# Kernel tuning notes

Hardware: AMD Instinct MI355X
Metric: run time of the kernel (lower is better)

Reference implementation:

```python
import jax, jax.numpy as jnp
import numpy as np

H, W, C_IN, C_ADD = 721, 1440, 78, 8
N_NODES, K = 5882, 128
DAY_OF_YEAR = 182.5  # module default time_of_year
LN_EPS = 1e-5        # haiku LayerNorm default
NORM_EPS = 1e-7


def setup_inputs() -> dict:
    key = jax.random.key(0)
    ks = jax.random.split(key, 4)
    return {
        "var_grid": jax.random.normal(ks[0], (H, W, C_IN), dtype=jnp.float32),
        "nearby_idx": jax.random.randint(ks[1], (N_NODES, K), 0, H * W),
        "input_means": jnp.zeros((C_IN + C_ADD,), jnp.float32),
        "input_stds": jnp.ones((C_IN + C_ADD,), jnp.float32),
        "W1": jax.random.normal(ks[2], (C_IN + C_ADD, 256), dtype=jnp.float32) * 0.1,
        "b1": jnp.zeros((256,), jnp.float32),
        "ln_scale": jnp.ones((256,), jnp.float32),
        "ln_offset": jnp.zeros((256,), jnp.float32),
        "W2": jax.random.normal(ks[3], (256, 256), dtype=jnp.float32) * 0.1,
        "b2": jnp.zeros((256,), jnp.float32),
    }


def _additional_features(h, w):
    # 8 extra channels: sin/cos of lat/lon, normalized day-of-year, 3 zero pads
    lat = jnp.linspace(-90.0, 90.0, h)
    lon = jnp.linspace(0.0, 360.0, w)
    lat2d = jnp.broadcast_to(lat[:, None], (h, w))
    lon2d = jnp.broadcast_to(lon[None, :], (h, w))
    lat_r, lon_r = jnp.radians(lat2d), jnp.radians(lon2d)
    day = jnp.float32(DAY_OF_YEAR / 365.0)
    z = jnp.zeros((h, w), jnp.float32)
    return jnp.stack([
        jnp.sin(lat_r), jnp.cos(lat_r), jnp.sin(lon_r), jnp.cos(lon_r),
        jnp.full((h, w), day, jnp.float32), z, z, z,
    ], axis=-1)  # [H, W, 8]


def reference(var_grid, nearby_idx, input_means, input_stds,
              W1, b1, ln_scale, ln_offset, W2, b2):
    h, w, c = var_grid.shape
    add = _additional_features(h, w)                       # [H, W, 8]
    flat = jnp.concatenate([var_grid, add], -1).reshape(h * w, c + C_ADD)
    gathered = flat[nearby_idx]                            # [N, K, 86] irregular gather
    x = (gathered - input_means) / (input_stds + NORM_EPS)
    hidden = jax.nn.relu(jnp.einsum('nkc,cd->nkd', x, W1) + b1)
    mu = hidden.mean(-1, keepdims=True)
    var = hidden.var(-1, keepdims=True)
    hidden = (hidden - mu) * jax.lax.rsqrt(var + LN_EPS) * ln_scale + ln_offset
    nodes = jnp.einsum('nkd,de->nke', hidden, W2) + b2     # [N, K, 256]
    return nodes
```

## Files before the change

kernel.cpp:

```cpp
#include <hip/hip_runtime.h>
#include <hip/hip_bf16.h>
#include <math.h>

#define GH 721
#define GW 1440
#define C_IN 78
#define NNODES 5882
#define KNEIGH 128
#define M_TOTAL (NNODES * KNEIGH)
#define TM 64
#define NBLOCKS (M_TOTAL / TM)

typedef __attribute__((ext_vector_type(8))) short bf16x8;
typedef __attribute__((ext_vector_type(4))) float f32x4;

__device__ __forceinline__ unsigned short f2bf(float x) {
    __hip_bfloat16 b = __float2bfloat16(x);
    union { __hip_bfloat16 h; unsigned short u; } cv; cv.h = b; return cv.u;
}

__global__ void prep_kernel(const float* __restrict__ W1, const float* __restrict__ W2,
                            const float* __restrict__ means, const float* __restrict__ stds,
                            const float* __restrict__ b1, const float* __restrict__ lnS,
                            const float* __restrict__ lnO, const float* __restrict__ b2,
                            unsigned short* __restrict__ bp1, unsigned short* __restrict__ bp2,
                            float* __restrict__ latT, float* __restrict__ lonT,
                            float* __restrict__ b1p, float* __restrict__ K1,
                            float* __restrict__ K2)
{
    const int NB1 = 3 * 4 * 256 * 8;
    const int NB2 = 8 * 4 * 256 * 8;
    const int NTOT = NB1 + NB2 + GH + GW + 256;
    for (int e = blockIdx.x * blockDim.x + threadIdx.x; e < NTOT;
         e += gridDim.x * blockDim.x) {
        if (e < NB1) {
            int j = e & 7, c = (e >> 3) & 255, o = (e >> 11) & 3, s = e >> 13;
            int k = s * 32 + o * 8 + j;
            float v = 0.f;
            if (k < 82) v = W1[k * 256 + c] / (stds[k] + 1e-7f);
            bp1[e] = f2bf(v);
        } else if (e < NB1 + NB2) {
            int t = e - NB1;
            int j = t & 7, c = (t >> 3) & 255, o = (t >> 11) & 3, s = t >> 13;
            int k = s * 32 + o * 8 + j;
            bp2[t] = f2bf(W2[k * 256 + c] * lnS[k]);
        } else if (e < NB1 + NB2 + GH) {
            int h = e - NB1 - NB2;
            float r = (-90.f + 0.25f * (float)h) * 0.017453292519943295f;
            latT[2 * h]     = sinf(r);
            latT[2 * h + 1] = cosf(r);
        } else if (e < NB1 + NB2 + GH + GW) {
            int w = e - NB1 - NB2 - GH;
            float r = ((float)w * (360.f / 1439.f)) * 0.017453292519943295f;
            lonT[2 * w]     = sinf(r);
            lonT[2 * w + 1] = cosf(r);
        } else {
            int c = e - NB1 - NB2 - GH - GW;
            float acc = b1[c];
            #pragma unroll 1
            for (int k = 0; k < 86; ++k) {
                float inv = 1.f / (stds[k] + 1e-7f);
                float w = W1[k * 256 + c] * inv;
                acc -= means[k] * w;
                if (k == 82) acc += 0.5f * w;
            }
            b1p[c] = acc;
            float k1 = 0.f, k2 = 0.f;
            #pragma unroll 1
            for (int k = 0; k < 256; ++k) {
                float w = W2[k * 256 + c];
                k1 += lnS[k] * w;
                k2 += lnO[k] * w;
            }
            K1[c] = k1;
            K2[c] = k2 + b2[c];
        }
    }
}

__global__ __launch_bounds__(512, 4)
void fused_kernel(const float* __restrict__ var_grid, const int* __restrict__ idxs,
                  const unsigned short* __restrict__ bp1, const unsigned short* __restrict__ bp2,
                  const float* __restrict__ latT, const float* __restrict__ lonT,
                  const float* __restrict__ b1p, const float* __restrict__ K1,
                  const float* __restrict__ K2,
                  float* __restrict__ out)
{
    __shared__ __align__(16) char smem[TM * 256 * 2];
    __shared__ float red[2][4][TM];
    unsigned short* h_lds = (unsigned short*)smem;
    unsigned short (*x_lds)[104] = (unsigned short (*)[104])smem;

    const int q_ = 1470, r_ = 4;
    const int xcd = blockIdx.x & 7;
    const int ii  = blockIdx.x >> 3;
    const int swz = (xcd < r_ ? xcd * (q_ + 1) : r_ * (q_ + 1) + (xcd - r_) * q_) + ii;

    const int tid  = threadIdx.x;
    const int lane = tid & 63;
    const int wave = tid >> 6;
    const int wr   = wave >> 2;
    const int wc   = wave & 3;
    const int l15  = lane & 15;
    const int lg   = lane >> 4;
    const int wbase = wc * 64;
    const int rbase = wr * 32;
    const long block0 = (long)swz * TM;

    {
        const int row = tid >> 3, p = tid & 7;
        const int idx = idxs[block0 + row];
        const int hh = idx / GW;
        const int ww = idx - hh * GW;
        const float* src = var_grid + (long)idx * C_IN;
        float2 g[5], tl, tl2;
        #pragma unroll
        for (int t = 0; t < 5; ++t) {
            const int q = p + 8 * t;
            if (q < 39) g[t] = *(const float2*)(src + 2 * q);
        }
        tl.x  = latT[2 * hh]; tl.y  = latT[2 * hh + 1];
        tl2.x = lonT[2 * ww]; tl2.y = lonT[2 * ww + 1];
        unsigned int* xrow = (unsigned int*)&x_lds[row][0];
        #pragma unroll
        for (int t = 0; t < 6; ++t) {
            const int q = p + 8 * t;
            float v0, v1;
            if (q < 39)      { v0 = g[t].x; v1 = g[t].y; }
            else if (q == 39){ v0 = tl.x;  v1 = tl.y; }
            else if (q == 40){ v0 = tl2.x; v1 = tl2.y; }
            else             { v0 = 0.f; v1 = 0.f; }
            xrow[q] = ((unsigned int)f2bf(v1) << 16) | (unsigned int)f2bf(v0);
        }
    }

    float b1v[4];
    #pragma unroll
    for (int nf = 0; nf < 4; ++nf) b1v[nf] = b1p[wbase + nf * 16 + l15];
    __syncthreads();

    f32x4 acc[2][4];
    #pragma unroll
    for (int mf = 0; mf < 2; ++mf)
        #pragma unroll
        for (int nf = 0; nf < 4; ++nf) acc[mf][nf] = (f32x4){0.f, 0.f, 0.f, 0.f};

    #pragma unroll
    for (int s = 0; s < 3; ++s) {
        bf16x8 af[2], bw[4];
        #pragma unroll
        for (int nf = 0; nf < 4; ++nf)
            bw[nf] = *(const bf16x8*)(bp1 + ((size_t)((s * 4 + lg) * 256) + wbase + nf * 16 + l15) * 8);
        #pragma unroll
        for (int mf = 0; mf < 2; ++mf)
            af[mf] = *(const bf16x8*)&x_lds[rbase + mf * 16 + l15][s * 32 + lg * 8];
        #pragma unroll
        for (int mf = 0; mf < 2; ++mf)
            #pragma unroll
            for (int nf = 0; nf < 4; ++nf)
                acc[mf][nf] = __builtin_amdgcn_mfma_f32_16x16x32_bf16(af[mf], bw[nf], acc[mf][nf], 0, 0, 0);
    }

    __syncthreads();

    float sm[2][4], sq[2][4];
    #pragma unroll
    for (int mf = 0; mf < 2; ++mf)
        #pragma unroll
        for (int i = 0; i < 4; ++i) { sm[mf][i] = 0.f; sq[mf][i] = 0.f; }

    #pragma unroll
    for (int mf = 0; mf < 2; ++mf)
        #pragma unroll
        for (int nf = 0; nf < 4; ++nf)
            #pragma unroll
            for (int i = 0; i < 4; ++i) {
                float v = fmaxf(acc[mf][nf][i] + b1v[nf], 0.f);
                sm[mf][i] += v;
                sq[mf][i] += v * v;
                int row = rbase + mf * 16 + lg * 4 + i;
                int col = wbase + nf * 16 + l15;
                unsigned off = (unsigned)(row * 512 + col * 2);
                off ^= (unsigned)((row & 7) << 4);
                *(unsigned short*)((char*)h_lds + off) = f2bf(v);
            }

    #pragma unroll
    for (int m = 1; m < 16; m <<= 1)
        #pragma unroll
        for (int mf = 0; mf < 2; ++mf)
            #pragma unroll
            for (int i = 0; i < 4; ++i) {
                sm[mf][i] += __shfl_xor(sm[mf][i], m, 64);
                sq[mf][i] += __shfl_xor(sq[mf][i], m, 64);
            }

    if (l15 == 0) {
        #pragma unroll
        for (int mf = 0; mf < 2; ++mf)
            #pragma unroll
            for (int i = 0; i < 4; ++i) {
                int row = rbase + mf * 16 + lg * 4 + i;
                red[0][wc][row] = sm[mf][i];
                red[1][wc][row] = sq[mf][i];
            }
    }
    __syncthreads();

    #pragma unroll
    for (int mf = 0; mf < 2; ++mf)
        #pragma unroll
        for (int nf = 0; nf < 4; ++nf) acc[mf][nf] = (f32x4){0.f, 0.f, 0.f, 0.f};

    #pragma unroll
    for (int s = 0; s < 8; ++s) {
        bf16x8 af[2], bw[4];
        #pragma unroll
        for (int nf = 0; nf < 4; ++nf)
            bw[nf] = *(const bf16x8*)(bp2 + ((size_t)((s * 4 + lg) * 256) + wbase + nf * 16 + l15) * 8);
        #pragma unroll
        for (int mf = 0; mf < 2; ++mf) {
            int row = rbase + mf * 16 + l15;
            unsigned off = (unsigned)(row * 512 + (s * 32 + lg * 8) * 2);
            off ^= (unsigned)((row & 7) << 4);
            af[mf] = *(const bf16x8*)((char*)h_lds + off);
        }
        #pragma unroll
        for (int mf = 0; mf < 2; ++mf)
            #pragma unroll
            for (int nf = 0; nf < 4; ++nf)
                acc[mf][nf] = __builtin_amdgcn_mfma_f32_16x16x32_bf16(af[mf], bw[nf], acc[mf][nf], 0, 0, 0);
    }

    float K1v[4], K2v[4];
    #pragma unroll
    for (int nf = 0; nf < 4; ++nf) {
        int col = wbase + nf * 16 + l15;
        K1v[nf] = K1[col]; K2v[nf] = K2[col];
    }
    #pragma unroll
    for (int mf = 0; mf < 2; ++mf)
        #pragma unroll
        for (int i = 0; i < 4; ++i) {
            int row = rbase + mf * 16 + lg * 4 + i;
            float tot = red[0][0][row] + red[0][1][row] + red[0][2][row] + red[0][3][row];
            float tq  = red[1][0][row] + red[1][1][row] + red[1][2][row] + red[1][3][row];
            float mean = tot * (1.f / 256.f);
            float var  = tq * (1.f / 256.f) - mean * mean;
            float rs = rsqrtf(var + 1e-5f);
            long row_g = block0 + row;
            float* po = out + row_g * 256 + wbase;
            #pragma unroll
            for (int nf = 0; nf < 4; ++nf)
                po[nf * 16 + l15] = rs * (acc[mf][nf][i] - mean * K1v[nf]) + K2v[nf];
        }
}

extern "C" void kernel_launch(void* const* d_in, const int* in_sizes, int n_in,
                              void* d_out, int out_size, void* d_ws, size_t ws_size,
                              hipStream_t stream) {
    const float* var_grid = (const float*)d_in[0];
    const int*   idxs     = (const int*)d_in[1];
    const float* means    = (const float*)d_in[2];
    const float* stds     = (const float*)d_in[3];
    const float* W1       = (const float*)d_in[4];
    const float* b1       = (const float*)d_in[5];
    const float* lnS      = (const float*)d_in[6];
    const float* lnO      = (const float*)d_in[7];
    const float* W2       = (const float*)d_in[8];
    const float* b2       = (const float*)d_in[9];
    float* out = (float*)d_out;

    char* ws = (char*)d_ws;
    unsigned short* bp1 = (unsigned short*)ws;
    unsigned short* bp2 = (unsigned short*)(ws + 49152);
    float* latT = (float*)(ws + 180224);
    float* lonT = (float*)(ws + 186000);
    float* b1p  = (float*)(ws + 197520);
    float* K1   = (float*)(ws + 198544);
    float* K2   = (float*)(ws + 199568);

    prep_kernel<<<362, 256, 0, stream>>>(W1, W2, means, stds, b1, lnS, lnO, b2,
                                         bp1, bp2, latT, lonT, b1p, K1, K2);
    fused_kernel<<<NBLOCKS, 512, 0, stream>>>(var_grid, idxs, bp1, bp2, latT, lonT,
                                              b1p, K1, K2, out);
}
```

Before: 427.6 us.

## Make fused kernel persistent over four tiles with double-buffered gather prefetch

Each block now handles four 64-row tiles instead of one, with the XCD swizzle constants updated for the smaller grid. The irregular gather for the next tile is issued into registers during the current tile's GEMMs and packed into a second x buffer. The aim is to hide gather latency behind MFMA work and amortize block launch and bias loads. The cost is more LDS (separate x, h and reduction buffers) and more live registers, which may lower occupancy under launch_bounds(512,4).

```diff
diff --git a/kernel.cpp b/kernel.cpp
--- a/kernel.cpp
+++ b/kernel.cpp
@@ -9,7 +9,8 @@
 #define KNEIGH 128
 #define M_TOTAL (NNODES * KNEIGH)
 #define TM 64
-#define NBLOCKS (M_TOTAL / TM)
+#define TILES 4
+#define NBLOCKS (M_TOTAL / (TM * TILES))
 
 typedef __attribute__((ext_vector_type(8))) short bf16x8;
 typedef __attribute__((ext_vector_type(4))) float f32x4;
@@ -86,12 +87,11 @@
                   const float* __restrict__ K2,
                   float* __restrict__ out)
 {
-    __shared__ __align__(16) char smem[TM * 256 * 2];
-    __shared__ float red[2][4][TM];
-    unsigned short* h_lds = (unsigned short*)smem;
-    unsigned short (*x_lds)[104] = (unsigned short (*)[104])smem;
-
-    const int q_ = 1470, r_ = 4;
+    __shared__ __align__(16) unsigned short x_lds[2][TM][104];
+    __shared__ __align__(16) unsigned short h_lds[TM * 256];
+    __shared__ float red[2][2][4][TM];
+
+    const int q_ = 367, r_ = 5;
     const int xcd = blockIdx.x & 7;
     const int ii  = blockIdx.x >> 3;
     const int swz = (xcd < r_ ? xcd * (q_ + 1) : r_ * (q_ + 1) + (xcd - r_) * q_) + ii;
@@ -105,155 +105,170 @@
     const int lg   = lane >> 4;
     const int wbase = wc * 64;
     const int rbase = wr * 32;
-    const long block0 = (long)swz * TM;
-
-    {
-        const int row = tid >> 3, p = tid & 7;
-        const int idx = idxs[block0 + row];
+    const long block0 = (long)swz * (TM * TILES);
+
+    const int grow = tid >> 3, gp = tid & 7;
+
+    float2 g[5], tl, tl2;
+
+    auto issue = [&](int t) {
+        const int idx = idxs[block0 + t * TM + grow];
         const int hh = idx / GW;
         const int ww = idx - hh * GW;
         const float* src = var_grid + (long)idx * C_IN;
-        float2 g[5], tl, tl2;
-        #pragma unroll
-        for (int t = 0; t < 5; ++t) {
-            const int q = p + 8 * t;
-            if (q < 39) g[t] = *(const float2*)(src + 2 * q);
+        #pragma unroll
+        for (int u = 0; u < 5; ++u) {
+            const int q = gp + 8 * u;
+            if (q < 39) g[u] = *(const float2*)(src + 2 * q);
         }
         tl.x  = latT[2 * hh]; tl.y  = latT[2 * hh + 1];
         tl2.x = lonT[2 * ww]; tl2.y = lonT[2 * ww + 1];
-        unsigned int* xrow = (unsigned int*)&x_lds[row][0];
-        #pragma unroll
-        for (int t = 0; t < 6; ++t) {
-            const int q = p + 8 * t;
+    };
+    auto pack = [&](int buf) {
+        unsigned int* xrow = (unsigned int*)&x_lds[buf][grow][0];
+        #pragma unroll
+        for (int u = 0; u < 6; ++u) {
+            const int q = gp + 8 * u;
             float v0, v1;
-            if (q < 39)      { v0 = g[t].x; v1 = g[t].y; }
-            else if (q == 39){ v0 = tl.x;  v1 = tl.y; }
-            else if (q == 40){ v0 = tl2.x; v1 = tl2.y; }
-            else             { v0 = 0.f; v1 = 0.f; }
+            if (q < 39)       { v0 = g[u].x; v1 = g[u].y; }
+            else if (q == 39) { v0 = tl.x;  v1 = tl.y; }
+            else if (q == 40) { v0 = tl2.x; v1 = tl2.y; }
+            else              { v0 = 0.f; v1 = 0.f; }
             xrow[q] = ((unsigned int)f2bf(v1) << 16) | (unsigned int)f2bf(v0);
         }
-    }
-
+    };
+
+    issue(0);
     float b1v[4];
     #pragma unroll
     for (int nf = 0; nf < 4; ++nf) b1v[nf] = b1p[wbase + nf * 16 + l15];
-    __syncthreads();
-
-    f32x4 acc[2][4];
+    pack(0);
+
     #pragma unroll
-    for (int mf = 0; mf < 2; ++mf)
-        #pragma unroll
-        for (int nf = 0; nf < 4; ++nf) acc[mf][nf] = (f32x4){0.f, 0.f, 0.f, 0.f};
-
-    #pragma unroll
-    for (int s = 0; s < 3; ++s) {
-        bf16x8 af[2], bw[4];
-        #pragma unroll
-        for (int nf = 0; nf < 4; ++nf)
-            bw[nf] = *(const bf16x8*)(bp1 + ((size_t)((s * 4 + lg) * 256) + wbase + nf * 16 + l15) * 8);
-        #pragma unroll
-        for (int mf = 0; mf < 2; ++mf)
-            af[mf] = *(const bf16x8*)&x_lds[rbase + mf * 16 + l15][s * 32 + lg * 8];
-        #pragma unroll
-        for (int mf = 0; mf < 2; ++mf)
+    for (int t = 0; t < TILES; ++t) {
+        __syncthreads();
+
+        if (t + 1 < TILES) issue(t + 1);
+
+        f32x4 acc[2][4];
+        #pragma unroll
+        for (int mf = 0; mf < 2; ++mf)
+            #pragma unroll
+            for (int nf = 0; nf < 4; ++nf) acc[mf][nf] = (f32x4){0.f, 0.f, 0.f, 0.f};
+
+        #pragma unroll
+        for (int s = 0; s < 3; ++s) {
+            bf16x8 af[2], bw[4];
             #pragma unroll
             for (int nf = 0; nf < 4; ++nf)
-                acc[mf][nf] = __builtin_amdgcn_mfma_f32_16x16x32_bf16(af[mf], bw[nf], acc[mf][nf], 0, 0, 0);
-    }
-
-    __syncthreads();
-
-    float sm[2][4], sq[2][4];
-    #pragma unroll
-    for (int mf = 0; mf < 2; ++mf)
-        #pragma unroll
-        for (int i = 0; i < 4; ++i) { sm[mf][i] = 0.f; sq[mf][i] = 0.f; }
-
-    #pragma unroll
-    for (int mf = 0; mf < 2; ++mf)
-        #pragma unroll
-        for (int nf = 0; nf < 4; ++nf)
-            #pragma unroll
-            for (int i = 0; i < 4; ++i) {
-                float v = fmaxf(acc[mf][nf][i] + b1v[nf], 0.f);
-                sm[mf][i] += v;
-                sq[mf][i] += v * v;
-                int row = rbase + mf * 16 + lg * 4 + i;
-                int col = wbase + nf * 16 + l15;
-                unsigned off = (unsigned)(row * 512 + col * 2);
+                bw[nf] = *(const bf16x8*)(bp1 + ((size_t)((s * 4 + lg) * 256) + wbase + nf * 16 + l15) * 8);
+            #pragma unroll
+            for (int mf = 0; mf < 2; ++mf)
+                af[mf] = *(const bf16x8*)&x_lds[t & 1][rbase + mf * 16 + l15][s * 32 + lg * 8];
+            #pragma unroll
+            for (int mf = 0; mf < 2; ++mf)
+                #pragma unroll
+                for (int nf = 0; nf < 4; ++nf)
+                    acc[mf][nf] = __builtin_amdgcn_mfma_f32_16x16x32_bf16(af[mf], bw[nf], acc[mf][nf], 0, 0, 0);
+        }
+
+        float sm[2][4], sq[2][4];
+        #pragma unroll
+        for (int mf = 0; mf < 2; ++mf)
+            #pragma unroll
+            for (int i = 0; i < 4; ++i) { sm[mf][i] = 0.f; sq[mf][i] = 0.f; }
+
+        #pragma unroll
+        for (int mf = 0; mf < 2; ++mf)
+            #pragma unroll
+            for (int nf = 0; nf < 4; ++nf)
+                #pragma unroll
+                for (int i = 0; i < 4; ++i) {
+                    float v = fmaxf(acc[mf][nf][i] + b1v[nf], 0.f);
+                    sm[mf][i] += v;
+                    sq[mf][i] += v * v;
+                    int row = rbase + mf * 16 + lg * 4 + i;
+                    int col = wbase + nf * 16 + l15;
+                    unsigned off = (unsigned)(row * 512 + col * 2);
+                    off ^= (unsigned)((row & 7) << 4);
+                    *(unsigned short*)((char*)h_lds + off) = f2bf(v);
+                }
+
+        #pragma unroll
+        for (int m = 1; m < 16; m <<= 1)
+            #pragma unroll
+            for (int mf = 0; mf < 2; ++mf)
+                #pragma unroll
+                for (int i = 0; i < 4; ++i) {
+                    sm[mf][i] += __shfl_xor(sm[mf][i], m, 64);
+                    sq[mf][i] += __shfl_xor(sq[mf][i], m, 64);
+                }
+
+        if (l15 == 0) {
+            #pragma unroll
+            for (int mf = 0; mf < 2; ++mf)
+                #pragma unroll
+                for (int i = 0; i < 4; ++i) {
+                    int row = rbase + mf * 16 + lg * 4 + i;
+                    red[t & 1][0][wc][row] = sm[mf][i];
+                    red[t & 1][1][wc][row] = sq[mf][i];
+                }
+        }
+
+        if (t + 1 < TILES) pack((t + 1) & 1);
+
+        __syncthreads();
+
+        #pragma unroll
+        for (int mf = 0; mf < 2; ++mf)
+            #pragma unroll
+            for (int nf = 0; nf < 4; ++nf) acc[mf][nf] = (f32x4){0.f, 0.f, 0.f, 0.f};
+
+        #pragma unroll
+        for (int s = 0; s < 8; ++s) {
+            bf16x8 af[2], bw[4];
+            #pragma unroll
+            for (int nf = 0; nf < 4; ++nf)
+                bw[nf] = *(const bf16x8*)(bp2 + ((size_t)((s * 4 + lg) * 256) + wbase + nf * 16 + l15) * 8);
+            #pragma unroll
+            for (int mf = 0; mf < 2; ++mf) {
+                int row = rbase + mf * 16 + l15;
+                unsigned off = (unsigned)(row * 512 + (s * 32 + lg * 8) * 2);
                 off ^= (unsigned)((row & 7) << 4);
-                *(unsigned short*)((char*)h_lds + off) = f2bf(v);
+                af[mf] = *(const bf16x8*)((char*)h_lds + off);
             }
-
-    #pragma unroll
-    for (int m = 1; m < 16; m <<= 1)
-        #pragma unroll
-        for (int mf = 0; mf < 2; ++mf)
-            #pragma unroll
-            for (int i = 0; i < 4; ++i) {
-                sm[mf][i] += __shfl_xor(sm[mf][i], m, 64);
-                sq[mf][i] += __shfl_xor(sq[mf][i], m, 64);
-            }
-
-    if (l15 == 0) {
+            #pragma unroll
+            for (int mf = 0; mf < 2; ++mf)
+                #pragma unroll
+                for (int nf = 0; nf < 4; ++nf)
+                    acc[mf][nf] = __builtin_amdgcn_mfma_f32_16x16x32_bf16(af[mf], bw[nf], acc[mf][nf], 0, 0, 0);
+        }
+
+        float K1v[4], K2v[4];
+        #pragma unroll
+        for (int nf = 0; nf < 4; ++nf) {
+            int col = wbase + nf * 16 + l15;
+            K1v[nf] = K1[col]; K2v[nf] = K2[col];
+        }
         #pragma unroll
         for (int mf = 0; mf < 2; ++mf)
             #pragma unroll
             for (int i = 0; i < 4; ++i) {
                 int row = rbase + mf * 16 + lg * 4 + i;
-                red[0][wc][row] = sm[mf][i];
-                red[1][wc][row] = sq[mf][i];
+                float tot = red[t & 1][0][0][row] + red[t & 1][0][1][row]
+                          + red[t & 1][0][2][row] + red[t & 1][0][3][row];
+                float tq  = red[t & 1][1][0][row] + red[t & 1][1][1][row]
+                          + red[t & 1][1][2][row] + red[t & 1][1][3][row];
+                float mean = tot * (1.f / 256.f);
+                float var  = tq * (1.f / 256.f) - mean * mean;
+                float rs = rsqrtf(var + 1e-5f);
+                long row_g = block0 + t * TM + row;
+                float* po = out + row_g * 256 + wbase;
+                #pragma unroll
+                for (int nf = 0; nf < 4; ++nf)
+                    po[nf * 16 + l15] = rs * (acc[mf][nf][i] - mean * K1v[nf]) + K2v[nf];
             }
     }
-    __syncthreads();
-
-    #pragma unroll
-    for (int mf = 0; mf < 2; ++mf)
-        #pragma unroll
-        for (int nf = 0; nf < 4; ++nf) acc[mf][nf] = (f32x4){0.f, 0.f, 0.f, 0.f};
-
-    #pragma unroll
-    for (int s = 0; s < 8; ++s) {
-        bf16x8 af[2], bw[4];
-        #pragma unroll
-        for (int nf = 0; nf < 4; ++nf)
-            bw[nf] = *(const bf16x8*)(bp2 + ((size_t)((s * 4 + lg) * 256) + wbase + nf * 16 + l15) * 8);
-        #pragma unroll
-        for (int mf = 0; mf < 2; ++mf) {
-            int row = rbase + mf * 16 + l15;
-            unsigned off = (unsigned)(row * 512 + (s * 32 + lg * 8) * 2);
-            off ^= (unsigned)((row & 7) << 4);
-            af[mf] = *(const bf16x8*)((char*)h_lds + off);
-        }
-        #pragma unroll
-        for (int mf = 0; mf < 2; ++mf)
-            #pragma unroll
-            for (int nf = 0; nf < 4; ++nf)
-                acc[mf][nf] = __builtin_amdgcn_mfma_f32_16x16x32_bf16(af[mf], bw[nf], acc[mf][nf], 0, 0, 0);
-    }
-
-    float K1v[4], K2v[4];
-    #pragma unroll
-    for (int nf = 0; nf < 4; ++nf) {
-        int col = wbase + nf * 16 + l15;
-        K1v[nf] = K1[col]; K2v[nf] = K2[col];
-    }
-    #pragma unroll
-    for (int mf = 0; mf < 2; ++mf)
-        #pragma unroll
-        for (int i = 0; i < 4; ++i) {
-            int row = rbase + mf * 16 + lg * 4 + i;
-            float tot = red[0][0][row] + red[0][1][row] + red[0][2][row] + red[0][3][row];
-            float tq  = red[1][0][row] + red[1][1][row] + red[1][2][row] + red[1][3][row];
-            float mean = tot * (1.f / 256.f);
-            float var  = tq * (1.f / 256.f) - mean * mean;
-            float rs = rsqrtf(var + 1e-5f);
-            long row_g = block0 + row;
-            float* po = out + row_g * 256 + wbase;
-            #pragma unroll
-            for (int nf = 0; nf < 4; ++nf)
-                po[nf * 16 + l15] = rs * (acc[mf][nf][i] - mean * K1v[nf]) + K2v[nf];
-        }
 }
 
 extern "C" void kernel_launch(void* const* d_in, const int* in_sizes, int n_in,
```

Result: slower. 909.3 us (+112.7%).

## Split gather into separate kernel writing bf16 staging buffer before MLP

Applied to the files above, without the earlier changes.

Splits the fused gather+MLP kernel into a standalone gather kernel and an MLP kernel. The gather kernel writes bf16 rows padded to 96 columns into a workspace buffer, and the MLP kernel reads its A operand straight from global memory. The intent is to decouple the latency-bound irregular gather from the MFMA compute. The cost is an extra round trip of about 144 MB through HBM. A fallback keeps the fused path when the workspace is too small.

```diff
diff --git a/kernel.cpp b/kernel.cpp
--- a/kernel.cpp
+++ b/kernel.cpp
@@ -8,8 +8,6 @@
 #define NNODES 5882
 #define KNEIGH 128
 #define M_TOTAL (NNODES * KNEIGH)
-#define TM 64
-#define NBLOCKS (M_TOTAL / TM)
 
 typedef __attribute__((ext_vector_type(8))) short bf16x8;
 typedef __attribute__((ext_vector_type(4))) float f32x4;
@@ -78,23 +76,63 @@
     }
 }
 
+__global__ __launch_bounds__(256)
+void gather_kernel(const float* __restrict__ var_grid, const int* __restrict__ idxs,
+                   const float* __restrict__ latT, const float* __restrict__ lonT,
+                   unsigned short* __restrict__ xbuf)
+{
+    const long NU = (long)M_TOTAL * 12;
+    const int b = blockIdx.x;
+    const int swz = (b & 7) * 256 + (b >> 3);
+    for (long unit = (long)swz * 256 + threadIdx.x; unit < NU;
+         unit += (long)gridDim.x * 256) {
+        const int row = (int)(unit / 12);
+        const int u   = (int)(unit - (long)row * 12);
+        const int idx = idxs[row];
+        const float* src = var_grid + (long)idx * C_IN;
+        float v[8];
+        if (u < 9) {
+            #pragma unroll
+            for (int j = 0; j < 4; ++j) {
+                float2 t = *(const float2*)(src + u * 8 + 2 * j);
+                v[2 * j] = t.x; v[2 * j + 1] = t.y;
+            }
+        } else if (u == 9) {
+            #pragma unroll
+            for (int j = 0; j < 3; ++j) {
+                float2 t = *(const float2*)(src + 72 + 2 * j);
+                v[2 * j] = t.x; v[2 * j + 1] = t.y;
+            }
+            int hh = idx / GW;
+            v[6] = latT[2 * hh]; v[7] = latT[2 * hh + 1];
+        } else if (u == 10) {
+            int hh = idx / GW;
+            int ww = idx - hh * GW;
+            v[0] = lonT[2 * ww]; v[1] = lonT[2 * ww + 1];
+            #pragma unroll
+            for (int j = 2; j < 8; ++j) v[j] = 0.f;
+        } else {
+            #pragma unroll
+            for (int j = 0; j < 8; ++j) v[j] = 0.f;
+        }
+        uint4 o;
+        o.x = ((unsigned)f2bf(v[1]) << 16) | f2bf(v[0]);
+        o.y = ((unsigned)f2bf(v[3]) << 16) | f2bf(v[2]);
+        o.z = ((unsigned)f2bf(v[5]) << 16) | f2bf(v[4]);
+        o.w = ((unsigned)f2bf(v[7]) << 16) | f2bf(v[6]);
+        *(uint4*)(xbuf + (size_t)row * 96 + u * 8) = o;
+    }
+}
+
 __global__ __launch_bounds__(512, 4)
-void fused_kernel(const float* __restrict__ var_grid, const int* __restrict__ idxs,
-                  const unsigned short* __restrict__ bp1, const unsigned short* __restrict__ bp2,
-                  const float* __restrict__ latT, const float* __restrict__ lonT,
-                  const float* __restrict__ b1p, const float* __restrict__ K1,
-                  const float* __restrict__ K2,
-                  float* __restrict__ out)
+void mlp_kernel(const unsigned short* __restrict__ xbuf,
+                const unsigned short* __restrict__ bp1, const unsigned short* __restrict__ bp2,
+                const float* __restrict__ b1p, const float* __restrict__ K1,
+                const float* __restrict__ K2,
+                float* __restrict__ out)
 {
-    __shared__ __align__(16) char smem[TM * 256 * 2];
-    __shared__ float red[2][4][TM];
-    unsigned short* h_lds = (unsigned short*)smem;
-    unsigned short (*x_lds)[104] = (unsigned short (*)[104])smem;
-
-    const int q_ = 1470, r_ = 4;
-    const int xcd = blockIdx.x & 7;
-    const int ii  = blockIdx.x >> 3;
-    const int swz = (xcd < r_ ? xcd * (q_ + 1) : r_ * (q_ + 1) + (xcd - r_) * q_) + ii;
+    __shared__ __align__(16) unsigned short h_lds[64 * 256];
+    __shared__ float red[2][4][64];
 
     const int tid  = threadIdx.x;
     const int lane = tid & 63;
@@ -105,7 +143,155 @@
     const int lg   = lane >> 4;
     const int wbase = wc * 64;
     const int rbase = wr * 32;
-    const long block0 = (long)swz * TM;
+    const long block0 = (long)blockIdx.x * 64;
+
+    float b1v[4];
+    #pragma unroll
+    for (int nf = 0; nf < 4; ++nf) b1v[nf] = b1p[wbase + nf * 16 + l15];
+
+    f32x4 acc[2][4];
+    #pragma unroll
+    for (int mf = 0; mf < 2; ++mf)
+        #pragma unroll
+        for (int nf = 0; nf < 4; ++nf) acc[mf][nf] = (f32x4){0.f, 0.f, 0.f, 0.f};
+
+    #pragma unroll
+    for (int s = 0; s < 3; ++s) {
+        bf16x8 af[2], bw[4];
+        #pragma unroll
+        for (int nf = 0; nf < 4; ++nf)
+            bw[nf] = *(const bf16x8*)(bp1 + ((size_t)((s * 4 + lg) * 256) + wbase + nf * 16 + l15) * 8);
+        #pragma unroll
+        for (int mf = 0; mf < 2; ++mf)
+            af[mf] = *(const bf16x8*)(xbuf + (size_t)(block0 + rbase + mf * 16 + l15) * 96
+                                            + s * 32 + lg * 8);
+        #pragma unroll
+        for (int mf = 0; mf < 2; ++mf)
+            #pragma unroll
+            for (int nf = 0; nf < 4; ++nf)
+                acc[mf][nf] = __builtin_amdgcn_mfma_f32_16x16x32_bf16(af[mf], bw[nf], acc[mf][nf], 0, 0, 0);
+    }
+
+    float sm[2][4], sq[2][4];
+    #pragma unroll
+    for (int mf = 0; mf < 2; ++mf)
+        #pragma unroll
+        for (int i = 0; i < 4; ++i) { sm[mf][i] = 0.f; sq[mf][i] = 0.f; }
+
+    #pragma unroll
+    for (int mf = 0; mf < 2; ++mf)
+        #pragma unroll
+        for (int nf = 0; nf < 4; ++nf)
+            #pragma unroll
+            for (int i = 0; i < 4; ++i) {
+                float v = fmaxf(acc[mf][nf][i] + b1v[nf], 0.f);
+                sm[mf][i] += v;
+                sq[mf][i] += v * v;
+                int row = rbase + mf * 16 + lg * 4 + i;
+                int col = wbase + nf * 16 + l15;
+                unsigned off = (unsigned)(row * 512 + col * 2);
+                off ^= (unsigned)((row & 7) << 4);
+                *(unsigned short*)((char*)h_lds + off) = f2bf(v);
+            }
+
+    #pragma unroll
+    for (int m = 1; m < 16; m <<= 1)
+        #pragma unroll
+        for (int mf = 0; mf < 2; ++mf)
+            #pragma unroll
+            for (int i = 0; i < 4; ++i) {
+                sm[mf][i] += __shfl_xor(sm[mf][i], m, 64);
+                sq[mf][i] += __shfl_xor(sq[mf][i], m, 64);
+            }
+
+    if (l15 == 0) {
+        #pragma unroll
+        for (int mf = 0; mf < 2; ++mf)
+            #pragma unroll
+            for (int i = 0; i < 4; ++i) {
+                int row = rbase + mf * 16 + lg * 4 + i;
+                red[0][wc][row] = sm[mf][i];
+                red[1][wc][row] = sq[mf][i];
+            }
+    }
+    __syncthreads();
+
+    #pragma unroll
+    for (int mf = 0; mf < 2; ++mf)
+        #pragma unroll
+        for (int nf = 0; nf < 4; ++nf) acc[mf][nf] = (f32x4){0.f, 0.f, 0.f, 0.f};
+
+    #pragma unroll
+    for (int s = 0; s < 8; ++s) {
+        bf16x8 af[2], bw[4];
+        #pragma unroll
+        for (int nf = 0; nf < 4; ++nf)
+            bw[nf] = *(const bf16x8*)(bp2 + ((size_t)((s * 4 + lg) * 256) + wbase + nf * 16 + l15) * 8);
+        #pragma unroll
+        for (int mf = 0; mf < 2; ++mf) {
+            int row = rbase + mf * 16 + l15;
+            unsigned off = (unsigned)(row * 512 + (s * 32 + lg * 8) * 2);
+            off ^= (unsigned)((row & 7) << 4);
+            af[mf] = *(const bf16x8*)((char*)h_lds + off);
+        }
+        #pragma unroll
+        for (int mf = 0; mf < 2; ++mf)
+            #pragma unroll
+            for (int nf = 0; nf < 4; ++nf)
+                acc[mf][nf] = __builtin_amdgcn_mfma_f32_16x16x32_bf16(af[mf], bw[nf], acc[mf][nf], 0, 0, 0);
+    }
+
+    float K1v[4], K2v[4];
+    #pragma unroll
+    for (int nf = 0; nf < 4; ++nf) {
+        int col = wbase + nf * 16 + l15;
+        K1v[nf] = K1[col]; K2v[nf] = K2[col];
+    }
+    #pragma unroll
+    for (int mf = 0; mf < 2; ++mf)
+        #pragma unroll
+        for (int i = 0; i < 4; ++i) {
+            int row = rbase + mf * 16 + lg * 4 + i;
+            float tot = red[0][0][row] + red[0][1][row] + red[0][2][row] + red[0][3][row];
+            float tq  = red[1][0][row] + red[1][1][row] + red[1][2][row] + red[1][3][row];
+            float mean = tot * (1.f / 256.f);
+            float var  = tq * (1.f / 256.f) - mean * mean;
+            float rs = rsqrtf(var + 1e-5f);
+            long row_g = block0 + row;
+            float* po = out + row_g * 256 + wbase;
+            #pragma unroll
+            for (int nf = 0; nf < 4; ++nf)
+                po[nf * 16 + l15] = rs * (acc[mf][nf][i] - mean * K1v[nf]) + K2v[nf];
+        }
+}
+
+__global__ __launch_bounds__(512, 4)
+void fused_fallback(const float* __restrict__ var_grid, const int* __restrict__ idxs,
+                    const unsigned short* __restrict__ bp1, const unsigned short* __restrict__ bp2,
+                    const float* __restrict__ latT, const float* __restrict__ lonT,
+                    const float* __restrict__ b1p, const float* __restrict__ K1,
+                    const float* __restrict__ K2,
+                    float* __restrict__ out)
+{
+    __shared__ __align__(16) unsigned short h_lds[64 * 256];
+    __shared__ float red[2][4][64];
+    unsigned short (*x_lds)[104] = (unsigned short (*)[104])h_lds;
+
+    const int q_ = 1470, r_ = 4;
+    const int xcd = blockIdx.x & 7;
+    const int ii  = blockIdx.x >> 3;
+    const int swz = (xcd < r_ ? xcd * (q_ + 1) : r_ * (q_ + 1) + (xcd - r_) * q_) + ii;
+
+    const int tid  = threadIdx.x;
+    const int lane = tid & 63;
+    const int wave = tid >> 6;
+    const int wr   = wave >> 2;
+    const int wc   = wave & 3;
+    const int l15  = lane & 15;
+    const int lg   = lane >> 4;
+    const int wbase = wc * 64;
+    const int rbase = wr * 32;
+    const long block0 = (long)swz * 64;
 
     {
         const int row = tid >> 3, p = tid & 7;
@@ -271,17 +457,36 @@
     const float* b2       = (const float*)d_in[9];
     float* out = (float*)d_out;
 
+    const size_t XBUF_BYTES = (size_t)M_TOTAL * 96 * 2;
     char* ws = (char*)d_ws;
-    unsigned short* bp1 = (unsigned short*)ws;
-    unsigned short* bp2 = (unsigned short*)(ws + 49152);
-    float* latT = (float*)(ws + 180224);
-    float* lonT = (float*)(ws + 186000);
-    float* b1p  = (float*)(ws + 197520);
-    float* K1   = (float*)(ws + 198544);
-    float* K2   = (float*)(ws + 199568);
-
-    prep_kernel<<<362, 256, 0, stream>>>(W1, W2, means, stds, b1, lnS, lnO, b2,
-                                         bp1, bp2, latT, lonT, b1p, K1, K2);
-    fused_kernel<<<NBLOCKS, 512, 0, stream>>>(var_grid, idxs, bp1, bp2, latT, lonT,
-                                              b1p, K1, K2, out);
-}
+
+    if (ws_size >= XBUF_BYTES + 262144) {
+        unsigned short* xbuf = (unsigned short*)ws;
+        char* aux = ws + XBUF_BYTES;
+        unsigned short* bp1 = (unsigned short*)aux;
+        unsigned short* bp2 = (unsigned short*)(aux + 49152);
+        float* latT = (float*)(aux + 180224);
+        float* lonT = (float*)(aux + 186000);
+        float* b1p  = (float*)(aux + 197520);
+        float* K1   = (float*)(aux + 198544);
+        float* K2   = (float*)(aux + 199568);
+
+        prep_kernel<<<362, 256, 0, stream>>>(W1, W2, means, stds, b1, lnS, lnO, b2,
+                                             bp1, bp2, latT, lonT, b1p, K1, K2);
+        gather_kernel<<<2048, 256, 0, stream>>>(var_grid, idxs, latT, lonT, xbuf);
+        mlp_kernel<<<M_TOTAL / 64, 512, 0, stream>>>(xbuf, bp1, bp2, b1p, K1, K2, out);
+    } else {
+        unsigned short* bp1 = (unsigned short*)ws;
+        unsigned short* bp2 = (unsigned short*)(ws + 49152);
+        float* latT = (float*)(ws + 180224);
+        float* lonT = (float*)(ws + 186000);
+        float* b1p  = (float*)(ws + 197520);
+        float* K1   = (float*)(ws + 198544);
+        float* K2   = (float*)(ws + 199568);
+
+        prep_kernel<<<362, 256, 0, stream>>>(W1, W2, means, stds, b1, lnS, lnO, b2,
+                                             bp1, bp2, latT, lonT, b1p, K1, K2);
+        fused_fallback<<<M_TOTAL / 64, 512, 0, stream>>>(var_grid, idxs, bp1, bp2,
+                                                         latT, lonT, b1p, K1, K2, out);
+    }
+}
```

New measurement: 525.4 us. 1.23x slower.
